# Optimization experiments

Hardware: AMD Instinct MI355X
Metric: run time of the kernel (lower is better)

## Reference

```python
import jax, jax.numpy as jnp
import numpy as np

D_MODEL = 1024
NHEAD = 16
HEAD_DIM = D_MODEL // NHEAD
ROPE_BASE = 10000.0


def rope_cos_sin(seq_len, dim, dtype=jnp.float32):
    inv_freq = 1.0 / (ROPE_BASE ** (jnp.arange(0, dim, 2, dtype=jnp.float32) / dim))
    t = jnp.arange(seq_len, dtype=jnp.float32)
    freqs = jnp.einsum('i,j->ij', t, inv_freq)        # [S, dim/2]
    emb = jnp.concatenate([freqs, freqs], axis=-1)    # [S, dim]
    return emb.astype(dtype), jnp.cos(emb).astype(dtype), jnp.sin(emb).astype(dtype)


def rotate_half(x):
    x1, x2 = jnp.split(x, 2, axis=-1)
    return jnp.concatenate([-x2, x1], axis=-1)


def setup_inputs() -> dict:
    key = jax.random.key(0)
    ks = jax.random.split(key, 11)
    B, S, D = 2, 2048, D_MODEL
    std = 1.0 / np.sqrt(D)
    return {
        'query': jax.random.normal(ks[0], (B, S, D), jnp.float32),
        'key_': jax.random.normal(ks[1], (B, S, D), jnp.float32),
        'value': jax.random.normal(ks[2], (B, S, D), jnp.float32),
        'Wq': jax.random.uniform(ks[3], (D, D), jnp.float32, -std, std),
        'bq': jax.random.uniform(ks[4], (D,), jnp.float32, -std, std),
        'Wk': jax.random.uniform(ks[5], (D, D), jnp.float32, -std, std),
        'bk': jax.random.uniform(ks[6], (D,), jnp.float32, -std, std),
        'Wv': jax.random.uniform(ks[7], (D, D), jnp.float32, -std, std),
        'bv': jax.random.uniform(ks[8], (D,), jnp.float32, -std, std),
        'Wo': jax.random.uniform(ks[9], (D, D), jnp.float32, -std, std),
        'bo': jax.random.uniform(ks[10], (D,), jnp.float32, -std, std),
    }


def reference(query, key_, value, Wq, bq, Wk, bk, Wv, bv, Wo, bo):
    B, T, D = query.shape
    S = key_.shape[1]
    H, Hd = NHEAD, HEAD_DIM
    scale = Hd ** -0.5
    # projections (torch Linear: x @ W^T + b), reshape to [B, H, L, Hd]
    q = (query @ Wq.T + bq).reshape(B, T, H, Hd).transpose(0, 2, 1, 3)
    k = (key_ @ Wk.T + bk).reshape(B, S, H, Hd).transpose(0, 2, 1, 3)
    v = (value @ Wv.T + bv).reshape(B, S, H, Hd).transpose(0, 2, 1, 3)
    # RoPE
    _, cos, sin = rope_cos_sin(max(T, S), Hd, query.dtype)
    cos_q, sin_q = cos[:T][None, None], sin[:S][None, None]
    q = q * cos_q + rotate_half(q) * sin_q
    k = k * cos_q + rotate_half(k) * sin_q
    # attention
    scores = jnp.einsum('bhtd,bhsd->bhts', q, k) * scale
    attn = jax.nn.softmax(scores, axis=-1)
    out = jnp.einsum('bhts,bhsd->bhtd', attn, v)
    out = out.transpose(0, 2, 1, 3).reshape(B, T, D)
    return out @ Wo.T + bo
```

## Files before the change

kernel.cpp:

```cpp
#include <hip/hip_runtime.h>
#include <hip/hip_bf16.h>
#include <math.h>

using bf16x8 = __attribute__((ext_vector_type(8))) short;
using f32x4  = __attribute__((ext_vector_type(4))) float;
using f32x16 = __attribute__((ext_vector_type(16))) float;

#define MFMA16(a,b,c) __builtin_amdgcn_mfma_f32_16x16x32_bf16(a,b,c,0,0,0)
#define MFMA32(a,b,c) __builtin_amdgcn_mfma_f32_32x32x16_bf16(a,b,c,0,0,0)

#define GLOAD_LDS16(g, s) __builtin_amdgcn_global_load_lds( \
    (const __attribute__((address_space(1))) unsigned int*)(const void*)(g), \
    (__attribute__((address_space(3))) unsigned int*)(void*)(s), 16, 0, 0)

static __device__ __forceinline__ short f2bf(float f) {
    __hip_bfloat16 h = __float2bfloat16(f);
    return *reinterpret_cast<short*>(&h);
}

static __device__ __forceinline__ int cvtpk(float lo, float hi) {
    int r;
    asm volatile("v_cvt_pk_bf16_f32 %0, %1, %2" : "=v"(r) : "v"(lo), "v"(hi));
    return r;
}

__global__ void prep_cast(const float* q, const float* k, const float* v,
                          const float* wq, const float* wk, const float* wv, const float* wo,
                          short* xq, short* xk, short* xv,
                          short* bwq, short* bwk, short* bwv, short* bwo) {
    const long NBIG = 1L << 20;
    const long NW   = 1L << 18;
    const long total = 3*NBIG + 4*NW;
    for (long i = (long)blockIdx.x*blockDim.x + threadIdx.x; i < total; i += (long)gridDim.x*blockDim.x) {
        const float* src; short* dst; long j = i;
        if (j < NBIG)              { src = q;  dst = xq;  }
        else if ((j -= NBIG) < NBIG) { src = k;  dst = xk;  }
        else if ((j -= NBIG) < NBIG) { src = v;  dst = xv;  }
        else if ((j -= NBIG) < NW)   { src = wq; dst = bwq; }
        else if ((j -= NW) < NW)     { src = wk; dst = bwk; }
        else if ((j -= NW) < NW)     { src = wv; dst = bwv; }
        else { j -= NW;              src = wo; dst = bwo; }
        float4 f = reinterpret_cast<const float4*>(src)[j];
        ushort4 o;
        o.x = (ushort)f2bf(f.x); o.y = (ushort)f2bf(f.y);
        o.z = (ushort)f2bf(f.z); o.w = (ushort)f2bf(f.w);
        reinterpret_cast<ushort4*>(dst)[j] = o;
    }
}

__global__ void rope_table(float* cost, float* sint) {
    int i = blockIdx.x*blockDim.x + threadIdx.x;
    int s = i >> 5, j = i & 31;
    double inv = pow(10000.0, -(double)j / 32.0);
    double a = (double)s * inv;
    cost[i] = (float)cos(a);
    sint[i] = (float)sin(a);
}

__device__ __forceinline__ void gemm_tile(const short* A, const short* B,
                                          int brow, int bcol, short* lds,
                                          f32x4 (&acc)[4][4]) {
    short* Al0 = lds;
    short* Al1 = lds + 4096;
    short* Bl0 = lds + 8192;
    short* Bl1 = lds + 12288;
    const int t = threadIdx.x;
    const int l = t & 63, qi = l & 15, h = l >> 4;
    const int w = t >> 6, wr = w >> 1, wc = w & 1;
    const f32x4 z4 = {0.f, 0.f, 0.f, 0.f};
#pragma unroll
    for (int i = 0; i < 4; ++i)
#pragma unroll
        for (int j = 0; j < 4; ++j) acc[i][j] = z4;

    const int srow = w*32 + (l >> 2);
    const int scol = (l & 3) << 3;
    const short* ga = A + (long)(brow + srow)*1024 + scol;
    const short* gb = B + (long)(bcol + srow)*1024 + scol;
    const int lo = w*32*32;

    GLOAD_LDS16(ga,            Al0 + lo);
    GLOAD_LDS16(ga + 16*1024,  Al0 + lo + 16*32);
    GLOAD_LDS16(gb,            Bl0 + lo);
    GLOAD_LDS16(gb + 16*1024,  Bl0 + lo + 16*32);
    asm volatile("s_waitcnt vmcnt(0)");
    __syncthreads();

    int cur = 0;
    for (int kt = 0; kt < 32; ++kt) {
        if (kt < 31) {
            short* An = cur ? Al0 : Al1;
            short* Bn = cur ? Bl0 : Bl1;
            GLOAD_LDS16(ga + ((kt+1) << 5),            An + lo);
            GLOAD_LDS16(ga + ((kt+1) << 5) + 16*1024,  An + lo + 16*32);
            GLOAD_LDS16(gb + ((kt+1) << 5),            Bn + lo);
            GLOAD_LDS16(gb + ((kt+1) << 5) + 16*1024,  Bn + lo + 16*32);
        }
        const short* Ac = cur ? Al1 : Al0;
        const short* Bc = cur ? Bl1 : Bl0;
        bf16x8 af[4], bfr[4];
#pragma unroll
        for (int mf = 0; mf < 4; ++mf)
            af[mf] = *(const bf16x8*)(Ac + (wr*64 + mf*16 + qi)*32 + h*8);
#pragma unroll
        for (int nf = 0; nf < 4; ++nf)
            bfr[nf] = *(const bf16x8*)(Bc + (wc*64 + nf*16 + qi)*32 + h*8);
        __builtin_amdgcn_s_setprio(1);
#pragma unroll
        for (int mf = 0; mf < 4; ++mf)
#pragma unroll
            for (int nf = 0; nf < 4; ++nf)
                acc[mf][nf] = MFMA16(af[mf], bfr[nf], acc[mf][nf]);
        __builtin_amdgcn_s_setprio(0);
        asm volatile("s_waitcnt vmcnt(0)");
        __syncthreads();
        cur ^= 1;
    }
}

__global__ __launch_bounds__(256, 3)
void gemm_qkv_kernel(const short* xq, const short* xk, const short* xv,
                     const short* wq, const short* wk, const short* wv,
                     const float* biq, const float* bik, const float* biv,
                     short* qo, short* ko, short* vo,
                     const float* cost, const float* sint) {
    __shared__ __align__(16) short lds[16384];
    const int mode = blockIdx.z;
    const short* A    = mode == 0 ? xq  : (mode == 1 ? xk  : xv);
    const short* B    = mode == 0 ? wq  : (mode == 1 ? wk  : wv);
    const float* bias = mode == 0 ? biq : (mode == 1 ? bik : biv);
    const int brow = blockIdx.x * 128, bcol = blockIdx.y * 128;
    f32x4 acc[4][4];
    gemm_tile(A, B, brow, bcol, lds, acc);

    const int t = threadIdx.x;
    const int l = t & 63, qi = l & 15, h = l >> 4;
    const int w = t >> 6, wr = w >> 1, wc = w & 1;
    const int n0 = bcol + wc*64, m0 = brow + wr*64;

    if (mode < 2) {
        short* dst = mode == 0 ? qo : ko;
        const float sc = (mode == 0) ? 0.125f : 1.0f;
#pragma unroll
        for (int nf = 0; nf < 2; ++nf) {
            const int j = nf*16 + qi;
            const float b0 = bias[n0 + nf*16 + qi];
            const float b1 = bias[n0 + (nf+2)*16 + qi];
#pragma unroll
            for (int mf = 0; mf < 4; ++mf) {
#pragma unroll
                for (int r = 0; r < 4; ++r) {
                    int m = m0 + mf*16 + 4*h + r;
                    int s = m & 2047;
                    float c  = cost[s*32 + j];
                    float si = sint[s*32 + j];
                    float x0 = acc[mf][nf  ][r] + b0;
                    float x1 = acc[mf][nf+2][r] + b1;
                    dst[(long)m*1024 + n0 + nf*16 + qi]      = f2bf((x0*c - x1*si) * sc);
                    dst[(long)m*1024 + n0 + (nf+2)*16 + qi]  = f2bf((x1*c + x0*si) * sc);
                }
            }
        }
    } else {
        __syncthreads();
        short* tb = lds + w*4096;
#pragma unroll
        for (int nf = 0; nf < 4; ++nf) {
            const int dl = nf*16 + qi;
            const float bb = bias[n0 + dl];
#pragma unroll
            for (int mf = 0; mf < 4; ++mf) {
#pragma unroll
                for (int r = 0; r < 4; ++r) {
                    const int sl = mf*16 + 4*h + r;
                    *(short*)((char*)tb + (((dl*64 + sl)*2) ^ ((dl & 7) << 4))) =
                        f2bf(acc[mf][nf][r] + bb);
                }
            }
        }
        const int hh2 = n0 >> 6;
        const int bb2 = m0 >> 11;
        const long s0g = (long)(m0 & 2047);
#pragma unroll
        for (int i = 0; i < 8; ++i) {
            const int c = l + (i << 6);
            const int dl = c >> 3, so = (c & 7) << 3;
            int4 vv = *(const int4*)((char*)tb + (((dl*64 + so)*2) ^ ((dl & 7) << 4)));
            *(int4*)(vo + (long)((bb2*16 + hh2)*64 + dl)*2048 + s0g + so) = vv;
        }
    }
}

__global__ __launch_bounds__(256, 3)
void gemm_o_kernel(const short* A, const short* B, const float* bias, float* out) {
    __shared__ __align__(16) short lds[16384];
    const int brow = blockIdx.x * 128, bcol = blockIdx.y * 128;
    f32x4 acc[4][4];
    gemm_tile(A, B, brow, bcol, lds, acc);
    const int t = threadIdx.x;
    const int l = t & 63, qi = l & 15, h = l >> 4;
    const int w = t >> 6, wr = w >> 1, wc = w & 1;
    const int n0 = bcol + wc*64, m0 = brow + wr*64;
#pragma unroll
    for (int nf = 0; nf < 4; ++nf) {
        float bb = bias[n0 + nf*16 + qi];
#pragma unroll
        for (int mf = 0; mf < 4; ++mf) {
#pragma unroll
            for (int r = 0; r < 4; ++r) {
                int m = m0 + mf*16 + 4*h + r;
                out[(long)m*1024 + n0 + nf*16 + qi] = acc[mf][nf][r] + bb;
            }
        }
    }
}

__global__ __launch_bounds__(256, 2)
void attn_kernel(const short* qw, const short* kw, const short* vtw, short* ow) {
    __shared__ __align__(16) short Kl[64*64];
    __shared__ __align__(16) short Vl[64*64];
    const int t = threadIdx.x;
    const int w = t >> 6, l = t & 63;
    const int q5 = l & 31, hi = l >> 5;
    const int b = blockIdx.z, hh = blockIdx.y;
    const long qrow = (long)b*2048 + blockIdx.x*128 + w*32 + q5;

    bf16x8 bqf[4];
#pragma unroll
    for (int s = 0; s < 4; ++s)
        bqf[s] = *(const bf16x8*)(qw + qrow*1024 + hh*64 + s*16 + hi*8);

    f32x16 o0, o1;
#pragma unroll
    for (int r = 0; r < 16; ++r) { o0[r] = 0.f; o1[r] = 0.f; }
    float mrun = -INFINITY, lrun = 0.f;

    const short* Kg = kw  + (long)b*2048*1024 + hh*64;
    const short* Vg = vtw + (long)(b*16 + hh)*64*2048;

    const int r0a = t >> 3,        e0a = (t & 7) << 3;
    const int r0b = (t+256) >> 3,  e0b = ((t+256) & 7) << 3;

    for (int jt = 0; jt < 32; ++jt) {
        __syncthreads();
        {
            int4 ka = *(const int4*)(Kg + (long)(jt*64 + r0a)*1024 + e0a);
            int4 va = *(const int4*)(Vg + (long)r0a*2048 + jt*64 + e0a);
            int4 kb = *(const int4*)(Kg + (long)(jt*64 + r0b)*1024 + e0b);
            int4 vb = *(const int4*)(Vg + (long)r0b*2048 + jt*64 + e0b);
            *(int4*)((char*)Kl + (((r0a*64 + e0a)*2) ^ ((r0a & 7) << 4))) = ka;
            *(int4*)((char*)Vl + (((r0a*64 + e0a)*2) ^ ((r0a & 7) << 4))) = va;
            *(int4*)((char*)Kl + (((r0b*64 + e0b)*2) ^ ((r0b & 7) << 4))) = kb;
            *(int4*)((char*)Vl + (((r0b*64 + e0b)*2) ^ ((r0b & 7) << 4))) = vb;
        }
        __syncthreads();

        f32x16 s0v, s1v;
#pragma unroll
        for (int r = 0; r < 16; ++r) { s0v[r] = 0.f; s1v[r] = 0.f; }
        __builtin_amdgcn_s_setprio(1);
#pragma unroll
        for (int s = 0; s < 4; ++s) {
            const int cb = (s*16 + hi*8) * 2;
            bf16x8 ka0 = *(const bf16x8*)((char*)Kl + (((q5*64*2) + cb) ^ ((q5 & 7) << 4)));
            bf16x8 ka1 = *(const bf16x8*)((char*)Kl + ((((32+q5)*64*2) + cb) ^ ((q5 & 7) << 4)));
            s0v = MFMA32(ka0, bqf[s], s0v);
            s1v = MFMA32(ka1, bqf[s], s1v);
        }
        __builtin_amdgcn_s_setprio(0);

        float tm = -INFINITY;
#pragma unroll
        for (int r = 0; r < 16; ++r) { tm = fmaxf(tm, s0v[r]); tm = fmaxf(tm, s1v[r]); }
        tm = fmaxf(tm, __shfl_xor(tm, 32));
        const float mnew = fmaxf(mrun, tm);
        const float corr = __expf(mrun - mnew);
        float ts = 0.f;
#pragma unroll
        for (int r = 0; r < 16; ++r) {
            s0v[r] = __expf(s0v[r] - mnew);
            s1v[r] = __expf(s1v[r] - mnew);
            ts += s0v[r] + s1v[r];
        }
        ts += __shfl_xor(ts, 32);
        lrun = lrun*corr + ts;
        mrun = mnew;
#pragma unroll
        for (int r = 0; r < 16; ++r) { o0[r] *= corr; o1[r] *= corr; }

        bf16x8 pf[4];
#pragma unroll
        for (int tt = 0; tt < 2; ++tt) {
#pragma unroll
            for (int ss = 0; ss < 2; ++ss) {
                const int base = 8*ss;
                float p0, p1, p2, p3, p4, p5, p6, p7;
                if (tt == 0) {
                    p0=s0v[base+0]; p1=s0v[base+1]; p2=s0v[base+2]; p3=s0v[base+3];
                    p4=s0v[base+4]; p5=s0v[base+5]; p6=s0v[base+6]; p7=s0v[base+7];
                } else {
                    p0=s1v[base+0]; p1=s1v[base+1]; p2=s1v[base+2]; p3=s1v[base+3];
                    p4=s1v[base+4]; p5=s1v[base+5]; p6=s1v[base+6]; p7=s1v[base+7];
                }
                int X0 = cvtpk(p0, p1), Y0 = cvtpk(p2, p3);
                int X1 = cvtpk(p4, p5), Y1 = cvtpk(p6, p7);
                int sx0 = __shfl_xor(X0, 32), sy0 = __shfl_xor(Y0, 32);
                int sx1 = __shfl_xor(X1, 32), sy1 = __shfl_xor(Y1, 32);
                union { int i[4]; bf16x8 v; } u;
                u.i[0] = hi ? sx1 : X0;
                u.i[1] = hi ? sy1 : Y0;
                u.i[2] = hi ? X1  : sx0;
                u.i[3] = hi ? Y1  : sy0;
                pf[2*tt + ss] = u.v;
            }
        }

        __builtin_amdgcn_s_setprio(1);
#pragma unroll
        for (int s4 = 0; s4 < 4; ++s4) {
            const int cb = (s4*16 + hi*8) * 2;
            bf16x8 va0 = *(const bf16x8*)((char*)Vl + (((q5*64*2) + cb) ^ ((q5 & 7) << 4)));
            bf16x8 va1 = *(const bf16x8*)((char*)Vl + ((((32+q5)*64*2) + cb) ^ ((q5 & 7) << 4)));
            o0 = MFMA32(va0, pf[s4], o0);
            o1 = MFMA32(va1, pf[s4], o1);
        }
        __builtin_amdgcn_s_setprio(0);
    }

    const float inv = 1.f / lrun;
    const long obase = qrow*1024 + hh*64;
#pragma unroll
    for (int dt = 0; dt < 2; ++dt) {
#pragma unroll
        for (int j = 0; j < 4; ++j) {
            ushort4 pk;
            if (dt == 0) {
                pk.x = (ushort)f2bf(o0[4*j+0]*inv); pk.y = (ushort)f2bf(o0[4*j+1]*inv);
                pk.z = (ushort)f2bf(o0[4*j+2]*inv); pk.w = (ushort)f2bf(o0[4*j+3]*inv);
            } else {
                pk.x = (ushort)f2bf(o1[4*j+0]*inv); pk.y = (ushort)f2bf(o1[4*j+1]*inv);
                pk.z = (ushort)f2bf(o1[4*j+2]*inv); pk.w = (ushort)f2bf(o1[4*j+3]*inv);
            }
            *(ushort4*)(ow + obase + dt*32 + 8*j + 4*hi) = pk;
        }
    }
}

extern "C" void kernel_launch(void* const* d_in, const int* in_sizes, int n_in,
                              void* d_out, int out_size, void* d_ws, size_t ws_size,
                              hipStream_t stream) {
    const float* query = (const float*)d_in[0];
    const float* key_  = (const float*)d_in[1];
    const float* value = (const float*)d_in[2];
    const float* Wq = (const float*)d_in[3];
    const float* bq = (const float*)d_in[4];
    const float* Wk = (const float*)d_in[5];
    const float* bk = (const float*)d_in[6];
    const float* Wv = (const float*)d_in[7];
    const float* bv = (const float*)d_in[8];
    const float* Wo = (const float*)d_in[9];
    const float* bo = (const float*)d_in[10];
    float* out = (float*)d_out;

    char* ws = (char*)d_ws;
    const size_t MB = 1u << 20;
    short* xq  = (short*)(ws);
    short* xk  = (short*)(ws + 8*MB);
    short* xv  = (short*)(ws + 16*MB);
    short* wqb = (short*)(ws + 24*MB);
    short* wkb = (short*)(ws + 26*MB);
    short* wvb = (short*)(ws + 28*MB);
    short* wob = (short*)(ws + 30*MB);
    short* qws = (short*)(ws + 32*MB);
    short* kws = (short*)(ws + 40*MB);
    short* vtw = (short*)(ws + 48*MB);
    float* cost = (float*)(ws + 56*MB);
    float* sint = (float*)(ws + 56*MB + 2048*32*4);
    short* attn = xq;

    hipLaunchKernelGGL(prep_cast, dim3(2048), dim3(256), 0, stream,
                       query, key_, value, Wq, Wk, Wv, Wo,
                       xq, xk, xv, wqb, wkb, wvb, wob);
    hipLaunchKernelGGL(rope_table, dim3(256), dim3(256), 0, stream, cost, sint);
    hipLaunchKernelGGL(gemm_qkv_kernel, dim3(32, 8, 3), dim3(256), 0, stream,
                       xq, xk, xv, wqb, wkb, wvb, bq, bk, bv,
                       qws, kws, vtw, cost, sint);
    hipLaunchKernelGGL(attn_kernel, dim3(16, 16, 2), dim3(256), 0, stream,
                       qws, kws, vtw, attn);
    hipLaunchKernelGGL(gemm_o_kernel, dim3(32, 8), dim3(256), 0, stream,
                       attn, wob, bo, out);
}
```

Baseline: 238.6 us.

## Fuse rope table into cast, remove attention LDS staging, use exp2 with lazy rescale

Folds the RoPE table computation into the cast kernel as extra blocks, dropping one launch. The attention kernel stops staging K/V tiles through LDS and its barriers; each lane loads its MFMA operands straight from global memory. Block IDs are remapped so that blocks sharing a head are grouped per XCD. Softmax switches to exp2 with log2(e) folded into the Q scale, and the running-max rescale is skipped while the max has grown by no more than 8. The trade-off is redundant global K/V loads across the 4 waves, which rely on L2 hits, plus a bounded risk that skipped rescales let unnormalised values grow.

```diff
diff --git a/kernel.cpp b/kernel.cpp
--- a/kernel.cpp
+++ b/kernel.cpp
@@ -27,11 +27,23 @@
 __global__ void prep_cast(const float* q, const float* k, const float* v,
                           const float* wq, const float* wk, const float* wv, const float* wo,
                           short* xq, short* xk, short* xv,
-                          short* bwq, short* bwk, short* bwv, short* bwo) {
+                          short* bwq, short* bwk, short* bwv, short* bwo,
+                          float* cost, float* sint) {
+    if (blockIdx.x >= 2048) {
+        int i = (blockIdx.x - 2048)*256*8 + threadIdx.x;
+        for (int rep = 0; rep < 8; ++rep, i += 256) {
+            int s = i >> 5, j = i & 31;
+            double inv = pow(10000.0, -(double)j / 32.0);
+            double a = (double)s * inv;
+            cost[i] = (float)cos(a);
+            sint[i] = (float)sin(a);
+        }
+        return;
+    }
     const long NBIG = 1L << 20;
     const long NW   = 1L << 18;
     const long total = 3*NBIG + 4*NW;
-    for (long i = (long)blockIdx.x*blockDim.x + threadIdx.x; i < total; i += (long)gridDim.x*blockDim.x) {
+    for (long i = (long)blockIdx.x*blockDim.x + threadIdx.x; i < total; i += 2048L*blockDim.x) {
         const float* src; short* dst; long j = i;
         if (j < NBIG)              { src = q;  dst = xq;  }
         else if ((j -= NBIG) < NBIG) { src = k;  dst = xk;  }
@@ -46,15 +58,6 @@
         o.z = (ushort)f2bf(f.z); o.w = (ushort)f2bf(f.w);
         reinterpret_cast<ushort4*>(dst)[j] = o;
     }
-}
-
-__global__ void rope_table(float* cost, float* sint) {
-    int i = blockIdx.x*blockDim.x + threadIdx.x;
-    int s = i >> 5, j = i & 31;
-    double inv = pow(10000.0, -(double)j / 32.0);
-    double a = (double)s * inv;
-    cost[i] = (float)cos(a);
-    sint[i] = (float)sin(a);
 }
 
 __device__ __forceinline__ void gemm_tile(const short* A, const short* B,
@@ -140,7 +143,7 @@
 
     if (mode < 2) {
         short* dst = mode == 0 ? qo : ko;
-        const float sc = (mode == 0) ? 0.125f : 1.0f;
+        const float sc = (mode == 0) ? 0.125f * 1.44269504088896f : 1.0f;
 #pragma unroll
         for (int nf = 0; nf < 2; ++nf) {
             const int j = nf*16 + qi;
@@ -217,13 +220,14 @@
 
 __global__ __launch_bounds__(256, 2)
 void attn_kernel(const short* qw, const short* kw, const short* vtw, short* ow) {
-    __shared__ __align__(16) short Kl[64*64];
-    __shared__ __align__(16) short Vl[64*64];
     const int t = threadIdx.x;
     const int w = t >> 6, l = t & 63;
     const int q5 = l & 31, hi = l >> 5;
-    const int b = blockIdx.z, hh = blockIdx.y;
-    const long qrow = (long)b*2048 + blockIdx.x*128 + w*32 + q5;
+    const int lid  = blockIdx.x + 16*blockIdx.y + 256*blockIdx.z;
+    const int wid  = ((lid & 7) << 6) | (lid >> 3);
+    const int qt   = wid & 15, bh = wid >> 4;
+    const int b    = bh >> 4,  hh = bh & 15;
+    const long qrow = (long)b*2048 + qt*128 + w*32 + q5;
 
     bf16x8 bqf[4];
 #pragma unroll
@@ -237,23 +241,19 @@
 
     const short* Kg = kw  + (long)b*2048*1024 + hh*64;
     const short* Vg = vtw + (long)(b*16 + hh)*64*2048;
-
-    const int r0a = t >> 3,        e0a = (t & 7) << 3;
-    const int r0b = (t+256) >> 3,  e0b = ((t+256) & 7) << 3;
+    const short* Kr0 = Kg + (long)q5*1024;
+    const short* Kr1 = Kg + (long)(32 + q5)*1024;
+    const short* Vr0 = Vg + (long)q5*2048;
+    const short* Vr1 = Vg + (long)(32 + q5)*2048;
 
     for (int jt = 0; jt < 32; ++jt) {
-        __syncthreads();
-        {
-            int4 ka = *(const int4*)(Kg + (long)(jt*64 + r0a)*1024 + e0a);
-            int4 va = *(const int4*)(Vg + (long)r0a*2048 + jt*64 + e0a);
-            int4 kb = *(const int4*)(Kg + (long)(jt*64 + r0b)*1024 + e0b);
-            int4 vb = *(const int4*)(Vg + (long)r0b*2048 + jt*64 + e0b);
-            *(int4*)((char*)Kl + (((r0a*64 + e0a)*2) ^ ((r0a & 7) << 4))) = ka;
-            *(int4*)((char*)Vl + (((r0a*64 + e0a)*2) ^ ((r0a & 7) << 4))) = va;
-            *(int4*)((char*)Kl + (((r0b*64 + e0b)*2) ^ ((r0b & 7) << 4))) = kb;
-            *(int4*)((char*)Vl + (((r0b*64 + e0b)*2) ^ ((r0b & 7) << 4))) = vb;
-        }
-        __syncthreads();
+        const int kvb = jt << 6;
+        bf16x8 vaf0[4], vaf1[4];
+#pragma unroll
+        for (int s4 = 0; s4 < 4; ++s4) {
+            vaf0[s4] = *(const bf16x8*)(Vr0 + kvb + s4*16 + hi*8);
+            vaf1[s4] = *(const bf16x8*)(Vr1 + kvb + s4*16 + hi*8);
+        }
 
         f32x16 s0v, s1v;
 #pragma unroll
@@ -261,9 +261,8 @@
         __builtin_amdgcn_s_setprio(1);
 #pragma unroll
         for (int s = 0; s < 4; ++s) {
-            const int cb = (s*16 + hi*8) * 2;
-            bf16x8 ka0 = *(const bf16x8*)((char*)Kl + (((q5*64*2) + cb) ^ ((q5 & 7) << 4)));
-            bf16x8 ka1 = *(const bf16x8*)((char*)Kl + ((((32+q5)*64*2) + cb) ^ ((q5 & 7) << 4)));
+            bf16x8 ka0 = *(const bf16x8*)(Kr0 + (long)kvb*1024 + s*16 + hi*8);
+            bf16x8 ka1 = *(const bf16x8*)(Kr1 + (long)kvb*1024 + s*16 + hi*8);
             s0v = MFMA32(ka0, bqf[s], s0v);
             s1v = MFMA32(ka1, bqf[s], s1v);
         }
@@ -273,20 +272,23 @@
 #pragma unroll
         for (int r = 0; r < 16; ++r) { tm = fmaxf(tm, s0v[r]); tm = fmaxf(tm, s1v[r]); }
         tm = fmaxf(tm, __shfl_xor(tm, 32));
-        const float mnew = fmaxf(mrun, tm);
-        const float corr = __expf(mrun - mnew);
+        if (!__all(tm - mrun <= 8.f)) {
+            const float mnew = fmaxf(mrun, tm);
+            const float corr = __builtin_amdgcn_exp2f(mrun - mnew);
+#pragma unroll
+            for (int r = 0; r < 16; ++r) { o0[r] *= corr; o1[r] *= corr; }
+            lrun *= corr;
+            mrun = mnew;
+        }
         float ts = 0.f;
 #pragma unroll
         for (int r = 0; r < 16; ++r) {
-            s0v[r] = __expf(s0v[r] - mnew);
-            s1v[r] = __expf(s1v[r] - mnew);
+            s0v[r] = __builtin_amdgcn_exp2f(s0v[r] - mrun);
+            s1v[r] = __builtin_amdgcn_exp2f(s1v[r] - mrun);
             ts += s0v[r] + s1v[r];
         }
         ts += __shfl_xor(ts, 32);
-        lrun = lrun*corr + ts;
-        mrun = mnew;
-#pragma unroll
-        for (int r = 0; r < 16; ++r) { o0[r] *= corr; o1[r] *= corr; }
+        lrun += ts;
 
         bf16x8 pf[4];
 #pragma unroll
@@ -318,11 +320,8 @@
         __builtin_amdgcn_s_setprio(1);
 #pragma unroll
         for (int s4 = 0; s4 < 4; ++s4) {
-            const int cb = (s4*16 + hi*8) * 2;
-            bf16x8 va0 = *(const bf16x8*)((char*)Vl + (((q5*64*2) + cb) ^ ((q5 & 7) << 4)));
-            bf16x8 va1 = *(const bf16x8*)((char*)Vl + ((((32+q5)*64*2) + cb) ^ ((q5 & 7) << 4)));
-            o0 = MFMA32(va0, pf[s4], o0);
-            o1 = MFMA32(va1, pf[s4], o1);
+            o0 = MFMA32(vaf0[s4], pf[s4], o0);
+            o1 = MFMA32(vaf1[s4], pf[s4], o1);
         }
         __builtin_amdgcn_s_setprio(0);
     }
@@ -378,10 +377,9 @@
     float* sint = (float*)(ws + 56*MB + 2048*32*4);
     short* attn = xq;
 
-    hipLaunchKernelGGL(prep_cast, dim3(2048), dim3(256), 0, stream,
+    hipLaunchKernelGGL(prep_cast, dim3(2080), dim3(256), 0, stream,
                        query, key_, value, Wq, Wk, Wv, Wo,
-                       xq, xk, xv, wqb, wkb, wvb, wob);
-    hipLaunchKernelGGL(rope_table, dim3(256), dim3(256), 0, stream, cost, sint);
+                       xq, xk, xv, wqb, wkb, wvb, wob, cost, sint);
     hipLaunchKernelGGL(gemm_qkv_kernel, dim3(32, 8, 3), dim3(256), 0, stream,
                        xq, xk, xv, wqb, wkb, wvb, bq, bk, bv,
                        qws, kws, vtw, cost, sint);
```

Result: slower. 291.5 us (+22.2%).
